# Kernel optimization log

Measured on AMD Instinct MI355X. Metric: run time of the kernel, lower is better.

## Reference

```python
import jax, jax.numpy as jnp
import numpy as np

N, M, D = 8192, 8192, 512

def setup_inputs() -> dict:
    key = jax.random.key(0)
    kx, ky = jax.random.split(key)
    X = jax.random.normal(kx, (N, D), dtype=jnp.float32)
    Y = jax.random.normal(ky, (M, D), dtype=jnp.float32)
    gamma = jnp.float32(1.0)  # learnable scalar kernel width
    return {"X": X, "Y": Y, "gamma": gamma}

def reference(X, Y, gamma):
    # RBF kernel: exp(-gamma * ||x_i - y_j||^2)
    x2 = jnp.sum(X * X, axis=-1)            # [n]
    y2 = jnp.sum(Y * Y, axis=-1)            # [m]
    xy = jnp.einsum('nd,md->nm', X, Y)      # [n, m] GEMM
    sq = x2[:, None] + y2[None, :] - 2.0 * xy
    sq = jnp.maximum(sq, 0.0)               # clamp tiny negatives from fp error
    return jnp.exp(-gamma * sq)
```

## Files before the change

### kernel.cpp

```cpp
#include <hip/hip_runtime.h>
#include <hip/hip_bf16.h>


#define N_ROWS 8192
#define D_DIM  512
#define BM 128
#define BN 128
#define BK 32

using bf16x8 = __attribute__((ext_vector_type(8))) short;
using f32x4  = __attribute__((ext_vector_type(4))) float;

__device__ inline unsigned pack2_bf16(float a, float b) {
    unsigned ua = __builtin_bit_cast(unsigned, a);
    unsigned ub = __builtin_bit_cast(unsigned, b);
    ua = (ua + 0x7fffu + ((ua >> 16) & 1u)) >> 16;
    ub = (ub + 0x7fffu + ((ub >> 16) & 1u)) >> 16;
    return ua | (ub << 16);
}

__global__ __launch_bounds__(64) void prep_kernel(const float* __restrict__ src,
                                                  unsigned short* __restrict__ dst,
                                                  float* __restrict__ norms) {
    const int row  = blockIdx.x;
    const int lane = threadIdx.x;
    const float4* s = reinterpret_cast<const float4*>(src) + (size_t)row * (D_DIM / 4);
    float4 v0 = s[lane * 2];
    float4 v1 = s[lane * 2 + 1];
    float ss = v0.x * v0.x + v0.y * v0.y + v0.z * v0.z + v0.w * v0.w +
               v1.x * v1.x + v1.y * v1.y + v1.z * v1.z + v1.w * v1.w;
    uint4 p;
    p.x = pack2_bf16(v0.x, v0.y);
    p.y = pack2_bf16(v0.z, v0.w);
    p.z = pack2_bf16(v1.x, v1.y);
    p.w = pack2_bf16(v1.z, v1.w);
    reinterpret_cast<uint4*>(dst + (size_t)row * D_DIM)[lane] = p;
    #pragma unroll
    for (int off = 32; off; off >>= 1) ss += __shfl_down(ss, off);
    if (lane == 0) norms[row] = ss;
}

__device__ inline void gload_lds16(const unsigned short* g, unsigned short* l) {
    __builtin_amdgcn_global_load_lds(
        (const __attribute__((address_space(1))) void*)g,
        (__attribute__((address_space(3))) void*)l, 16, 0, 0);
}

__global__ __launch_bounds__(256, 2) void rbf_gemm(
    const unsigned short* __restrict__ Xb, const unsigned short* __restrict__ Yb,
    const float* __restrict__ x2, const float* __restrict__ y2,
    const float* __restrict__ gptr, float* __restrict__ out) {
    __shared__ unsigned short sA[BM * BK];
    __shared__ unsigned short sB[BN * BK];

    const int bid  = blockIdx.x;
    const int swz  = (bid & 7) * 512 + (bid >> 3);
    const int brow = swz >> 6;
    const int bcol = swz & 63;

    const int tid  = threadIdx.x;
    const int lane = tid & 63;
    const int wid  = tid >> 6;
    const int wr   = wid >> 1;
    const int wc   = wid & 1;

    f32x4 acc[4][4] = {};

    const unsigned short* gA =
        Xb + (size_t)(brow * BM + wid * 32 + (lane >> 2)) * D_DIM + (lane & 3) * 8;
    const unsigned short* gB =
        Yb + (size_t)(bcol * BN + wid * 32 + (lane >> 2)) * D_DIM + (lane & 3) * 8;
    unsigned short* lA = sA + (wid * 32) * BK;
    unsigned short* lB = sB + (wid * 32) * BK;

    const bf16x8* ra = reinterpret_cast<const bf16x8*>(
        sA + (wr * 64 + (lane & 15)) * BK + (lane >> 4) * 8);
    const bf16x8* rb = reinterpret_cast<const bf16x8*>(
        sB + (wc * 64 + (lane & 15)) * BK + (lane >> 4) * 8);

    for (int kt = 0; kt < D_DIM / BK; ++kt) {
        const unsigned short* ga = gA + kt * BK;
        const unsigned short* gb = gB + kt * BK;
        #pragma unroll
        for (int j = 0; j < 2; ++j) {
            gload_lds16(ga + j * 16 * D_DIM, lA + j * 16 * BK);
            gload_lds16(gb + j * 16 * D_DIM, lB + j * 16 * BK);
        }
        __syncthreads();

        bf16x8 a[4], b[4];
        #pragma unroll
        for (int m = 0; m < 4; ++m) a[m] = ra[m * 64];
        #pragma unroll
        for (int n = 0; n < 4; ++n) b[n] = rb[n * 64];
        #pragma unroll
        for (int m = 0; m < 4; ++m)
            #pragma unroll
            for (int n = 0; n < 4; ++n)
                acc[m][n] = __builtin_amdgcn_mfma_f32_16x16x32_bf16(a[m], b[n], acc[m][n], 0, 0, 0);
        __syncthreads();
    }

    const float g = *gptr;
    const int rbase = brow * BM + wr * 64 + ((lane >> 4) << 2);
    const int cbase = bcol * BN + wc * 64 + (lane & 15);

    float yv[4];
    #pragma unroll
    for (int n = 0; n < 4; ++n) yv[n] = y2[cbase + n * 16];
    float xv[4][4];
    #pragma unroll
    for (int m = 0; m < 4; ++m)
        #pragma unroll
        for (int r = 0; r < 4; ++r) xv[m][r] = x2[rbase + m * 16 + r];

    #pragma unroll
    for (int m = 0; m < 4; ++m) {
        #pragma unroll
        for (int r = 0; r < 4; ++r) {
            const size_t rowoff = (size_t)(rbase + m * 16 + r) * N_ROWS;
            #pragma unroll
            for (int n = 0; n < 4; ++n) {
                float sq = xv[m][r] + yv[n] - 2.0f * acc[m][n][r];
                sq = fmaxf(sq, 0.0f);
                out[rowoff + cbase + n * 16] = __expf(-g * sq);
            }
        }
    }
}

extern "C" void kernel_launch(void* const* d_in, const int* in_sizes, int n_in,
                              void* d_out, int out_size, void* d_ws, size_t ws_size,
                              hipStream_t stream) {
    const float* X = (const float*)d_in[0];
    const float* Y = (const float*)d_in[1];
    const float* gamma = (const float*)d_in[2];
    float* out = (float*)d_out;

    unsigned short* Xb = (unsigned short*)d_ws;
    unsigned short* Yb = Xb + (size_t)N_ROWS * D_DIM;
    float* x2 = (float*)(Yb + (size_t)N_ROWS * D_DIM);
    float* y2 = x2 + N_ROWS;

    prep_kernel<<<N_ROWS, 64, 0, stream>>>(X, Xb, x2);
    prep_kernel<<<N_ROWS, 64, 0, stream>>>(Y, Yb, y2);

    const int grid = (N_ROWS / BM) * (N_ROWS / BN);
    rbf_gemm<<<grid, 256, 0, stream>>>(Xb, Yb, x2, y2, gamma, out);
}
```

Before: 353.9 us.

## Use 256x256 tiles with double-buffered LDS, XOR swizzle and phased MFMA schedule

Grows the GEMM tile to 256x256 with BK=64 and 512 threads, so each 8-wave block does more MFMA work per staged byte. LDS is double-buffered, and global-to-LDS loads for the next k-tile are issued in four quarters interleaved with four MFMA phases, using explicit vmcnt waits, barriers and setprio. An XOR swizzle on the LDS column layout is meant to avoid bank conflicts. The cost is higher register pressure (128 accumulator floats per lane) and 128KB of LDS per block, which may limit occupancy. With only 1024 blocks, wave quantization across the CUs is also a risk.

```diff
diff --git a/kernel.cpp b/kernel.cpp
--- a/kernel.cpp
+++ b/kernel.cpp
@@ -2,11 +2,12 @@
 #include <hip/hip_bf16.h>
 
 
-#define N_ROWS 8192
-#define D_DIM  512
-#define BM 128
-#define BN 128
-#define BK 32
+#define NROWS 8192
+#define D_DIM 512
+#define BM 256
+#define BN 256
+#define BK 64
+#define NKT (D_DIM / BK)
 
 using bf16x8 = __attribute__((ext_vector_type(8))) short;
 using f32x4  = __attribute__((ext_vector_type(4))) float;
@@ -46,84 +47,153 @@
         (__attribute__((address_space(3))) void*)l, 16, 0, 0);
 }
 
-__global__ __launch_bounds__(256, 2) void rbf_gemm(
+__global__ __launch_bounds__(512, 2) void rbf_gemm(
     const unsigned short* __restrict__ Xb, const unsigned short* __restrict__ Yb,
     const float* __restrict__ x2, const float* __restrict__ y2,
     const float* __restrict__ gptr, float* __restrict__ out) {
-    __shared__ unsigned short sA[BM * BK];
-    __shared__ unsigned short sB[BN * BK];
+    __shared__ unsigned short sA[2][BM * BK];
+    __shared__ unsigned short sB[2][BN * BK];
 
     const int bid  = blockIdx.x;
-    const int swz  = (bid & 7) * 512 + (bid >> 3);
-    const int brow = swz >> 6;
-    const int bcol = swz & 63;
+    const int swz  = (bid & 7) * 128 + (bid >> 3);
+    const int brow = swz >> 5;
+    const int bcol = swz & 31;
 
     const int tid  = threadIdx.x;
     const int lane = tid & 63;
     const int wid  = tid >> 6;
-    const int wr   = wid >> 1;
-    const int wc   = wid & 1;
-
-    f32x4 acc[4][4] = {};
-
-    const unsigned short* gA =
-        Xb + (size_t)(brow * BM + wid * 32 + (lane >> 2)) * D_DIM + (lane & 3) * 8;
-    const unsigned short* gB =
-        Yb + (size_t)(bcol * BN + wid * 32 + (lane >> 2)) * D_DIM + (lane & 3) * 8;
-    unsigned short* lA = sA + (wid * 32) * BK;
-    unsigned short* lB = sB + (wid * 32) * BK;
-
-    const bf16x8* ra = reinterpret_cast<const bf16x8*>(
-        sA + (wr * 64 + (lane & 15)) * BK + (lane >> 4) * 8);
-    const bf16x8* rb = reinterpret_cast<const bf16x8*>(
-        sB + (wc * 64 + (lane & 15)) * BK + (lane >> 4) * 8);
-
-    for (int kt = 0; kt < D_DIM / BK; ++kt) {
-        const unsigned short* ga = gA + kt * BK;
-        const unsigned short* gb = gB + kt * BK;
-        #pragma unroll
-        for (int j = 0; j < 2; ++j) {
-            gload_lds16(ga + j * 16 * D_DIM, lA + j * 16 * BK);
-            gload_lds16(gb + j * 16 * D_DIM, lB + j * 16 * BK);
-        }
-        __syncthreads();
-
-        bf16x8 a[4], b[4];
-        #pragma unroll
-        for (int m = 0; m < 4; ++m) a[m] = ra[m * 64];
-        #pragma unroll
-        for (int n = 0; n < 4; ++n) b[n] = rb[n * 64];
-        #pragma unroll
-        for (int m = 0; m < 4; ++m)
-            #pragma unroll
-            for (int n = 0; n < 4; ++n)
-                acc[m][n] = __builtin_amdgcn_mfma_f32_16x16x32_bf16(a[m], b[n], acc[m][n], 0, 0, 0);
-        __syncthreads();
+    const int wr   = wid >> 2;
+    const int wc   = wid & 3;
+
+    const int srow = tid >> 3;
+    const int scol = ((tid & 7) ^ ((tid >> 3) & 7)) * 8;
+    const unsigned short* gA0 = Xb + (size_t)(brow * BM) * D_DIM + scol;
+    const unsigned short* gB0 = Yb + (size_t)(bcol * BN) * D_DIM + scol;
+
+    const int lr = lane & 15;
+    const int kg = lane >> 4;
+    const int lx = lane & 7;
+    const int sl0 = ((0 * 4 + kg) ^ lx) * 8;
+    const int sl1 = ((1 * 4 + kg) ^ lx) * 8;
+    const int aBase = (wr * 128 + lr) * BK;
+    const int bBase = (wc * 64 + lr) * BK;
+
+    f32x4 acc[8][4] = {};
+    bf16x8 av[4][2], bv[4][2];
+
+    auto STAGE = [&](int d, int kt, int q) {
+        const bool isA = q >= 2;
+        const int half = q & 1;
+        const unsigned short* g = (isA ? gA0 : gB0) +
+            (size_t)(half * 128 + srow) * D_DIM + kt * BK;
+        unsigned short* l = (isA ? sA[d] : sB[d]) +
+            (half * 128 + srow) * BK + (tid & 7) * 8;
+        gload_lds16(g, l);
+        gload_lds16(g + 64 * D_DIM, l + 64 * BK);
+    };
+
+    #define LDF(p) (*reinterpret_cast<const bf16x8*>(p))
+    #define MFMA(a, b, c) __builtin_amdgcn_mfma_f32_16x16x32_bf16(a, b, c, 0, 0, 0)
+
+    #pragma unroll
+    for (int q = 0; q < 4; ++q) STAGE(0, 0, q);
+
+    for (int t = 0; t < NKT; ++t) {
+        const int c = t & 1, d = c ^ 1;
+        const bool pre = (t + 1 < NKT);
+        const unsigned short* A = sA[c];
+        const unsigned short* B = sB[c];
+
+        if (pre) STAGE(d, t + 1, 0);
+        if (pre) asm volatile("s_waitcnt vmcnt(2)" ::: "memory");
+        else     asm volatile("s_waitcnt vmcnt(0)" ::: "memory");
+        asm volatile("s_barrier" ::: "memory");
+        #pragma unroll
+        for (int m = 0; m < 4; ++m) {
+            av[m][0] = LDF(A + aBase + m * 16 * BK + sl0);
+            av[m][1] = LDF(A + aBase + m * 16 * BK + sl1);
+        }
+        #pragma unroll
+        for (int n = 0; n < 2; ++n) {
+            bv[n][0] = LDF(B + bBase + n * 16 * BK + sl0);
+            bv[n][1] = LDF(B + bBase + n * 16 * BK + sl1);
+        }
+        __builtin_amdgcn_s_setprio(1);
+        #pragma unroll
+        for (int m = 0; m < 4; ++m)
+            #pragma unroll
+            for (int n = 0; n < 2; ++n) {
+                acc[m][n] = MFMA(av[m][0], bv[n][0], acc[m][n]);
+                acc[m][n] = MFMA(av[m][1], bv[n][1], acc[m][n]);
+            }
+        __builtin_amdgcn_s_setprio(0);
+        asm volatile("s_barrier" ::: "memory");
+
+        if (pre) STAGE(d, t + 1, 1);
+        #pragma unroll
+        for (int n = 2; n < 4; ++n) {
+            bv[n][0] = LDF(B + bBase + n * 16 * BK + sl0);
+            bv[n][1] = LDF(B + bBase + n * 16 * BK + sl1);
+        }
+        __builtin_amdgcn_s_setprio(1);
+        #pragma unroll
+        for (int m = 0; m < 4; ++m)
+            #pragma unroll
+            for (int n = 2; n < 4; ++n) {
+                acc[m][n] = MFMA(av[m][0], bv[n][0], acc[m][n]);
+                acc[m][n] = MFMA(av[m][1], bv[n][1], acc[m][n]);
+            }
+        __builtin_amdgcn_s_setprio(0);
+        asm volatile("s_barrier" ::: "memory");
+
+        if (pre) STAGE(d, t + 1, 2);
+        #pragma unroll
+        for (int m = 0; m < 4; ++m) {
+            av[m][0] = LDF(A + aBase + (m + 4) * 16 * BK + sl0);
+            av[m][1] = LDF(A + aBase + (m + 4) * 16 * BK + sl1);
+        }
+        __builtin_amdgcn_s_setprio(1);
+        #pragma unroll
+        for (int m = 0; m < 4; ++m)
+            #pragma unroll
+            for (int n = 0; n < 2; ++n) {
+                acc[m + 4][n] = MFMA(av[m][0], bv[n][0], acc[m + 4][n]);
+                acc[m + 4][n] = MFMA(av[m][1], bv[n][1], acc[m + 4][n]);
+            }
+        __builtin_amdgcn_s_setprio(0);
+        asm volatile("s_barrier" ::: "memory");
+
+        if (pre) STAGE(d, t + 1, 3);
+        __builtin_amdgcn_s_setprio(1);
+        #pragma unroll
+        for (int m = 0; m < 4; ++m)
+            #pragma unroll
+            for (int n = 2; n < 4; ++n) {
+                acc[m + 4][n] = MFMA(av[m][0], bv[n][0], acc[m + 4][n]);
+                acc[m + 4][n] = MFMA(av[m][1], bv[n][1], acc[m + 4][n]);
+            }
+        __builtin_amdgcn_s_setprio(0);
+        asm volatile("s_barrier" ::: "memory");
     }
 
     const float g = *gptr;
-    const int rbase = brow * BM + wr * 64 + ((lane >> 4) << 2);
-    const int cbase = bcol * BN + wc * 64 + (lane & 15);
+    const int rbase = brow * BM + wr * 128 + (kg << 2);
+    const int cbase = bcol * BN + wc * 64 + lr;
 
     float yv[4];
     #pragma unroll
     for (int n = 0; n < 4; ++n) yv[n] = y2[cbase + n * 16];
-    float xv[4][4];
-    #pragma unroll
-    for (int m = 0; m < 4; ++m)
-        #pragma unroll
-        for (int r = 0; r < 4; ++r) xv[m][r] = x2[rbase + m * 16 + r];
-
-    #pragma unroll
-    for (int m = 0; m < 4; ++m) {
+
+    #pragma unroll
+    for (int m = 0; m < 8; ++m) {
         #pragma unroll
         for (int r = 0; r < 4; ++r) {
-            const size_t rowoff = (size_t)(rbase + m * 16 + r) * N_ROWS;
+            const float xr = x2[rbase + m * 16 + r];
+            const size_t ro = (size_t)(rbase + m * 16 + r) * NROWS + cbase;
             #pragma unroll
             for (int n = 0; n < 4; ++n) {
-                float sq = xv[m][r] + yv[n] - 2.0f * acc[m][n][r];
-                sq = fmaxf(sq, 0.0f);
-                out[rowoff + cbase + n * 16] = __expf(-g * sq);
+                float sq = fmaxf(xr + yv[n] - 2.0f * acc[m][n][r], 0.0f);
+                out[ro + n * 16] = __expf(-g * sq);
             }
         }
     }
@@ -138,13 +208,13 @@
     float* out = (float*)d_out;
 
     unsigned short* Xb = (unsigned short*)d_ws;
-    unsigned short* Yb = Xb + (size_t)N_ROWS * D_DIM;
-    float* x2 = (float*)(Yb + (size_t)N_ROWS * D_DIM);
-    float* y2 = x2 + N_ROWS;
-
-    prep_kernel<<<N_ROWS, 64, 0, stream>>>(X, Xb, x2);
-    prep_kernel<<<N_ROWS, 64, 0, stream>>>(Y, Yb, y2);
-
-    const int grid = (N_ROWS / BM) * (N_ROWS / BN);
-    rbf_gemm<<<grid, 256, 0, stream>>>(Xb, Yb, x2, y2, gamma, out);
-}
+    unsigned short* Yb = Xb + (size_t)NROWS * D_DIM;
+    float* x2 = (float*)(Yb + (size_t)NROWS * D_DIM);
+    float* y2 = x2 + NROWS;
+
+    prep_kernel<<<NROWS, 64, 0, stream>>>(X, Xb, x2);
+    prep_kernel<<<NROWS, 64, 0, stream>>>(Y, Yb, y2);
+
+    const int grid = (NROWS / BM) * (NROWS / BN);
+    rbf_gemm<<<grid, 512, 0, stream>>>(Xb, Yb, x2, y2, gamma, out);
+}
```

New measurement: 364.8 us. 1.03x slower.
